# Optimization experiments

Hardware: AMD Instinct MI355X
Metric: run time of the kernel (lower is better)

Reference implementation:

```python
import jax, jax.numpy as jnp
import numpy as np

B, D, H, L = 2, 1024, 16, 4
BLK = 16                 # block_size == max_text_tokens
MT, MF = 16, 2032        # max_text_tokens, max_font_tokens
S = MT + MF              # 2048
NB = S // BLK            # 128 blocks
V = 490                  # font_vocab_size
HD = D // H              # 64
WIN = 30                 # 3*max_glyph_tokens/block_size = 3*160/16
NGLOB, NRAND = 1, 2      # BigBird global / random blocks
SOS = 0.42


def _make_layout():
    # Deterministic BigBird block layout per head: [H, NB, NB] bool
    rng = np.random.default_rng(0)
    layout = np.zeros((H, NB, NB), dtype=bool)
    layout[:, :NGLOB, :] = True          # global rows
    layout[:, :, :NGLOB] = True          # global cols
    for i in range(NB):                  # sliding window
        layout[:, i, max(0, i - WIN // 2):min(NB, i + WIN // 2 + 1)] = True
    for h in range(H):                   # random blocks
        for i in range(NB):
            layout[h, i, rng.choice(NB, size=NRAND, replace=False)] = True
    return jnp.asarray(layout)


def setup_inputs() -> dict:
    key = jax.random.key(0)
    ks = jax.random.split(key, 16)
    p = lambda k, shape: (0.02 * jax.random.normal(k, shape)).astype(jnp.float32)
    return {
        "text_embeddings": jax.random.normal(ks[0], (B, MT, D), jnp.float32),
        "font_embeddings": jax.random.normal(ks[1], (B, MF, D), jnp.float32),
        "layout": _make_layout(),
        "Wq": p(ks[2], (L, D, D)), "bq": jnp.zeros((L, D), jnp.float32),
        "Wk": p(ks[3], (L, D, D)), "bk": jnp.zeros((L, D), jnp.float32),
        "Wv": p(ks[4], (L, D, D)), "bv": jnp.zeros((L, D), jnp.float32),
        "Wo": p(ks[5], (L, D, D)), "bo": jnp.zeros((L, D), jnp.float32),
        "ln1_g": jnp.ones((L, D), jnp.float32), "ln1_b": jnp.zeros((L, D), jnp.float32),
        "ln2_g": jnp.ones((L, D), jnp.float32), "ln2_b": jnp.zeros((L, D), jnp.float32),
        "W1": p(ks[6], (L, D, 4 * D)), "b1": jnp.zeros((L, 4 * D), jnp.float32),
        "W2": p(ks[7], (L, 4 * D, D)), "b2": jnp.zeros((L, D), jnp.float32),
        "lnf_g": jnp.ones((D,), jnp.float32), "lnf_b": jnp.zeros((D,), jnp.float32),
        "Wout": p(ks[8], (D, V)),
    }


def _ln(x, g, b, eps=1e-5):
    mu = x.mean(-1, keepdims=True)
    var = ((x - mu) ** 2).mean(-1, keepdims=True)
    return (x - mu) * jax.lax.rsqrt(var + eps) * g + b


def _forward(text_embeddings, font_embeddings, layout, Wq, bq, Wk, bk, Wv, bv, Wo, bo,
             ln1_g, ln1_b, ln2_g, ln2_b, W1, b1, W2, b2, lnf_g, lnf_b, Wout):
    sos = jnp.full((B, 1, D), SOS, text_embeddings.dtype)
    x = jnp.concatenate([sos, text_embeddings, font_embeddings[:, :-1, :]], axis=1)  # [B,S,D]
    # token-level mask = block-sparse BigBird layout AND causal -> [H,S,S]
    tok_mask = jnp.repeat(jnp.repeat(layout, BLK, axis=1), BLK, axis=2)
    tok_mask = tok_mask & jnp.tril(jnp.ones((S, S), bool))[None]
    neg = jnp.asarray(-1e9, x.dtype)
    scale = jnp.asarray(1.0 / np.sqrt(HD), x.dtype)

    def layer(x, p):
        wq, bq_, wk, bk_, wv, bv_, wo, bo_, g1, gb1, g2, gb2, w1, bb1, w2, bb2 = p
        q = (x @ wq + bq_).reshape(B, S, H, HD).transpose(0, 2, 1, 3)
        k = (x @ wk + bk_).reshape(B, S, H, HD).transpose(0, 2, 1, 3)
        v = (x @ wv + bv_).reshape(B, S, H, HD).transpose(0, 2, 1, 3)
        scores = jnp.einsum('bhqd,bhkd->bhqk', q, k) * scale
        scores = jnp.where(tok_mask[None], scores, neg)
        probs = jax.nn.softmax(scores, axis=-1)
        a = jnp.einsum('bhqk,bhkd->bhqd', probs, v).transpose(0, 2, 1, 3).reshape(B, S, D)
        a = a @ wo + bo_
        x = _ln(x + a, g1, gb1)                                   # post-norm residual
        m = jax.nn.gelu(x @ w1 + bb1, approximate=False) @ w2 + bb2  # dropout=eval no-op
        x = _ln(x + m, g2, gb2)
        return x, None

    params = (Wq, bq, Wk, bk, Wv, bv, Wo, bo, ln1_g, ln1_b, ln2_g, ln2_b, W1, b1, W2, b2)
    x, _ = jax.lax.scan(jax.checkpoint(layer), x, params)
    logits = _ln(x, lnf_g, lnf_b) @ Wout                          # [B,S,V]
    return logits[:, :MT, :], logits[:, MT:, :]


def reference(text_embeddings, font_embeddings, layout, Wq, bq, Wk, bk, Wv, bv, Wo, bo,
              ln1_g, ln1_b, ln2_g, ln2_b, W1, b1, W2, b2, lnf_g, lnf_b, Wout):
    return _forward(text_embeddings, font_embeddings, layout, Wq, bq, Wk, bk, Wv, bv, Wo, bo,
                    ln1_g, ln1_b, ln2_g, ln2_b, W1, b1, W2, b2, lnf_g, lnf_b, Wout)
```

## Files before the change

### kernel.cpp

```cpp
#include <hip/hip_runtime.h>
#include <hip/hip_bf16.h>
#include <math.h>


typedef __hip_bfloat16 bf16;
typedef __attribute__((ext_vector_type(8))) short bf16x8;
typedef __attribute__((ext_vector_type(8))) unsigned short us8;
typedef __attribute__((ext_vector_type(4))) unsigned short us4;
typedef __attribute__((ext_vector_type(4))) float f32x4;
typedef __attribute__((ext_vector_type(8))) _Float16 f16x8;

#define S_LEN 2048
#define D_MODEL 1024
#define NBLK 128
#define NHEAD 16
#define BATCH 2
#define M_ROWS 4096
#define VOCAB 490

__device__ __forceinline__ float ldw(const void* p, size_t i, bool bf) {
    return bf ? __bfloat162float(((const bf16*)p)[i]) : ((const float*)p)[i];
}
__device__ __forceinline__ bool is_bf(const unsigned* probe) {
    return probe[0] != 0x3F800000u;
}
__device__ __forceinline__ unsigned short f2b(float f) {
    union { float f; unsigned u; } x; x.f = f;
    return (unsigned short)((x.u + 0x7FFFu + ((x.u >> 16) & 1u)) >> 16);
}
__device__ __forceinline__ unsigned short f2h(float f) {
    union { _Float16 h; unsigned short u; } x; x.h = (_Float16)f;
    return x.u;
}
__device__ __forceinline__ unsigned packh(float a, float b) {
    return (unsigned)f2h(a) | ((unsigned)f2h(b) << 16);
}
__device__ __forceinline__ float gelu_exact(float v) {
    float z = fabsf(v) * 0.70710678118654752f;
    float t = __builtin_amdgcn_rcpf(fmaf(0.3275911f, z, 1.f));
    float p = t * fmaf(t, fmaf(t, fmaf(t, fmaf(t, 1.061405429f, -1.453152027f),
                  1.421413741f), -0.284496736f), 0.254829592f);
    float er = 1.f - p * __expf(-z * z);
    er = copysignf(er, v);
    return 0.5f * v * (1.f + er);
}

__global__ __launch_bounds__(256) void norm_layout_kernel(
    const unsigned char* __restrict__ lraw, unsigned char* __restrict__ mask)
{
    int i = blockIdx.x * 256 + threadIdx.x;
    bool bytes_mode = (lraw[1] == 1);
    unsigned char v;
    if (bytes_mode) v = lraw[i] ? 1 : 0;
    else            v = ((const unsigned*)lraw)[i] ? 1 : 0;
    mask[i] = v;
}

__global__ __launch_bounds__(256) void build_x_kernel(
    const void* __restrict__ text, const void* __restrict__ font,
    float* __restrict__ x, unsigned short* __restrict__ xb,
    const unsigned* __restrict__ probe)
{
    bool bf = is_bf(probe);
    size_t idx = (size_t)blockIdx.x * 256 + threadIdx.x;
    int d = (int)(idx & 1023);
    int s = (int)((idx >> 10) & 2047);
    int b = (int)(idx >> 21);
    float v;
    if (s == 0)       v = bf ? 0.419921875f : 0.42f;
    else if (s <= 16) v = ldw(text, ((size_t)(b * 16 + (s - 1))) * 1024 + d, bf);
    else              v = ldw(font, ((size_t)(b * 2032 + (s - 17))) * 1024 + d, bf);
    x[idx] = v;
    xb[idx] = f2b(v);
}

__device__ __forceinline__ void transw_tile(
    const void* W, size_t wOff, unsigned short* Wt,
    int K, int N, int k0, int n0, int t, bool bf)
{
    __shared__ unsigned short tile[32][36];
    int r  = t >> 3;
    int c4 = (t & 7) * 4;
    int n = n0 + c4;
    us4 tv;
    if (n + 4 <= N) {
        if (bf) {
            tv = *(const us4*)((const unsigned short*)W + wOff + (size_t)(k0 + r) * N + n);
        } else {
            float4 f = *(const float4*)((const float*)W + wOff + (size_t)(k0 + r) * N + n);
            tv = (us4){ f2b(f.x), f2b(f.y), f2b(f.z), f2b(f.w) };
        }
    } else {
        #pragma unroll
        for (int i = 0; i < 4; ++i)
            tv[i] = (n + i < N) ? f2b(ldw(W, wOff + (size_t)(k0 + r) * N + n + i, bf))
                                : (unsigned short)0;
    }
    *(us4*)(&tile[r][c4]) = tv;
    __syncthreads();
    int rn = t >> 3;
    int k4 = (t & 7) * 4;
    us4 ov = { tile[k4 + 0][rn], tile[k4 + 1][rn], tile[k4 + 2][rn], tile[k4 + 3][rn] };
    *(us4*)(&Wt[(size_t)(n0 + rn) * K + k0 + k4]) = ov;
}

__global__ __launch_bounds__(256) void transw_kernel(
    const void* __restrict__ W, size_t wOff, unsigned short* __restrict__ Wt,
    int K, int N, const unsigned* __restrict__ probe)
{
    transw_tile(W, wOff, Wt, K, N, blockIdx.x * 32, blockIdx.y * 32,
                threadIdx.x, is_bf(probe));
}

__global__ __launch_bounds__(256) void transw_layer_kernel(
    const void* __restrict__ Wq, const void* __restrict__ Wk,
    const void* __restrict__ Wv, const void* __restrict__ Wo,
    const void* __restrict__ W1, const void* __restrict__ W2,
    size_t wo4, size_t wo16, unsigned short* __restrict__ wt,
    const unsigned* __restrict__ probe)
{
    bool bf = is_bf(probe);
    const size_t M1 = (size_t)1 << 20;
    int bx = blockIdx.x, by = blockIdx.y, z = blockIdx.z;
    if (z == 0) {
        int wsel = by >> 5;
        const void* W = wsel == 0 ? Wq : (wsel == 1 ? Wk : (wsel == 2 ? Wv : Wo));
        transw_tile(W, wo4, wt + (size_t)wsel * M1, 1024, 1024,
                    bx * 32, (by & 31) * 32, threadIdx.x, bf);
    } else if (z == 1) {
        transw_tile(W1, wo16, wt + 4 * M1, 1024, 4096,
                    bx * 32, by * 32, threadIdx.x, bf);
    } else {
        transw_tile(W2, wo16, wt + 8 * M1, 4096, 1024,
                    by * 32, bx * 32, threadIdx.x, bf);
    }
}

__global__ __launch_bounds__(512) void gemm_kernel(
    const unsigned short* __restrict__ Ab,
    const unsigned short* __restrict__ Wt, size_t wtStride,
    const void* __restrict__ b0, const void* __restrict__ b1p, const void* __restrict__ b2p,
    size_t bOff,
    float* __restrict__ C0, float* __restrict__ C1, float* __restrict__ C2,
    void* __restrict__ Cb0, void* __restrict__ Cb1, void* __restrict__ Cb2,
    float* __restrict__ Cp,
    int M, int N, int K, int act, int outmode, const unsigned* __restrict__ probe)
{
    bool bf = is_bf(probe);
    __shared__ __align__(16) unsigned short As[2][128 * 64];
    __shared__ __align__(16) unsigned short Bs[2][128 * 64];

    int t    = threadIdx.x;
    int lane = t & 63;
    int wid  = t >> 6;
    int wm   = wid >> 2;
    int wn   = wid & 3;

    int gx  = gridDim.x;
    int gy  = gridDim.y;
    int bid = blockIdx.y * gx + blockIdx.x;
    int mi, ni;
    if (gy == 32 && (gx & 3) == 0) {
        int xcd = bid & 7, c = bid >> 3;
        int xr = xcd >> 2, xc = xcd & 3;
        int rw = gx >> 2;
        mi = xr * 16 + (c & 15);
        ni = xc * rw + (c >> 4);
    } else {
        int nwg = gx * gy;
        int swz = (bid & 7) * (nwg >> 3) + (bid >> 3);
        mi = swz / gx; ni = swz % gx;
    }
    int m0  = mi * 128;
    int n0t = ni * 128;
    int sel = n0t / N;
    int n0  = n0t - sel * N;
    int zz  = blockIdx.z;
    int Kit = K / gridDim.z;
    int kbase = zz * Kit;

    const void* bias = sel == 0 ? b0 : (sel == 1 ? b1p : b2p);
    float* C         = sel == 0 ? C0 : (sel == 1 ? C1 : C2);
    void* Cb         = sel == 0 ? Cb0 : (sel == 1 ? Cb1 : Cb2);
    const unsigned short* Wtb = Wt + (size_t)sel * wtStride;
    const bool vtr = (outmode == 3 && sel == 2);

    f32x4 acc[4][2];
    #pragma unroll
    for (int i = 0; i < 4; i++)
        #pragma unroll
        for (int j = 0; j < 2; j++)
            acc[i][j] = (f32x4){0.f, 0.f, 0.f, 0.f};

    const int fm = lane & 15;

    auto stageA = [&](int bb, int kt) {
        int k0 = kbase + (kt << 6);
        #pragma unroll
        for (int c = 0; c < 2; ++c) {
            int p    = (wid * 2 + c) * 64 + lane;
            int row  = p >> 3;
            int cp   = p & 7;
            int csrc = cp ^ (row & 7);
            const unsigned short* src = Ab + (size_t)(m0 + row) * K + k0 + csrc * 8;
            unsigned short* dst = &As[bb][(wid * 2 + c) * 512];
            __builtin_amdgcn_global_load_lds(
                (const __attribute__((address_space(1))) unsigned int*)src,
                (__attribute__((address_space(3))) unsigned int*)dst, 16, 0, 0);
        }
    };
    auto stageB = [&](int bb, int kt) {
        int k0 = kbase + (kt << 6);
        #pragma unroll
        for (int c = 0; c < 2; ++c) {
            int p    = (wid * 2 + c) * 64 + lane;
            int row  = p >> 3;
            int cp   = p & 7;
            int csrc = cp ^ (row & 7);
            const unsigned short* src = Wtb + (size_t)(n0 + row) * K + k0 + csrc * 8;
            unsigned short* dst = &Bs[bb][(wid * 2 + c) * 512];
            __builtin_amdgcn_global_load_lds(
                (const __attribute__((address_space(1))) unsigned int*)src,
                (__attribute__((address_space(3))) unsigned int*)dst, 16, 0, 0);
        }
    };
    auto compute = [&](int bb) {
        #pragma unroll
        for (int kk = 0; kk < 2; ++kk) {
            int cq = kk * 4 + (lane >> 4);
            bf16x8 af[4], bfr[2];
            #pragma unroll
            for (int i = 0; i < 4; ++i) {
                int r = wm * 64 + i * 16 + fm;
                af[i] = *(const bf16x8*)(&As[bb][r * 64 + (cq ^ (r & 7)) * 8]);
            }
            #pragma unroll
            for (int j = 0; j < 2; ++j) {
                int n = wn * 32 + j * 16 + fm;
                bfr[j] = *(const bf16x8*)(&Bs[bb][n * 64 + (cq ^ (n & 7)) * 8]);
            }
            #pragma unroll
            for (int i = 0; i < 4; ++i)
                #pragma unroll
                for (int j = 0; j < 2; ++j)
                    acc[i][j] = __builtin_amdgcn_mfma_f32_16x16x32_bf16(
                        af[i], bfr[j], acc[i][j], 0, 0, 0);
        }
    };

    int nt = Kit >> 6;
    stageA(0, 0);
    stageB(0, 0);
    __syncthreads();

    for (int kt = 0; kt < nt; ++kt) {
        int cur = kt & 1;
        bool more = (kt + 1) < nt;
        if (more) { stageA(cur ^ 1, kt + 1); stageB(cur ^ 1, kt + 1); }
        compute(cur);
        __syncthreads();
    }

    int rq = (lane >> 4) * 4;
    #pragma unroll
    for (int j = 0; j < 2; ++j) {
        int n = n0 + wn * 32 + j * 16 + fm;
        if (n >= N) continue;
        float bv = (bias && zz == 0) ? ldw(bias, bOff + n, bf) : 0.f;
        #pragma unroll
        for (int i = 0; i < 4; ++i) {
            int mb = m0 + wm * 64 + i * 16 + rq;
            if (zz > 0) {
                #pragma unroll
                for (int r = 0; r < 4; ++r)
                    Cp[(size_t)(mb + r) * N + n] = acc[i][j][r];
                continue;
            }
            if (vtr) {
                us4 o;
                #pragma unroll
                for (int r = 0; r < 4; ++r) o[r] = f2h(acc[i][j][r] + bv);
                int bb2 = mb >> 11, s0 = mb & 2047, hh = n >> 6, dd = n & 63;
                *(us4*)(&((unsigned short*)Cb)[((((size_t)(bb2 * 16 + hh)) * 64 + dd) << 11) + s0]) = o;
                continue;
            }
            #pragma unroll
            for (int r = 0; r < 4; ++r) {
                int m = mb + r;
                float v = acc[i][j][r] + bv;
                if (act == 1) v = gelu_exact(v);
                if (outmode == 0) {
                    C[(size_t)m * N + n] = v;
                } else if (outmode == 2) {
                    ((unsigned short*)Cb)[(size_t)m * N + n] = f2b(v);
                } else if (outmode == 3) {
                    ((unsigned short*)Cb)[(size_t)m * N + n] = f2h(v);
                } else {
                    int b = m >> 11;
                    int s = m & 2047;
                    size_t dst;
                    if (s < 16) dst = ((size_t)(b * 16 + s)) * N + n;
                    else        dst = (size_t)(BATCH * 16) * N + ((size_t)(b * 2032 + (s - 16))) * N + n;
                    if (bf) ((unsigned short*)Cb)[dst] = f2b(v);
                    else    ((float*)Cb)[dst] = v;
                }
            }
        }
    }
}

__global__ __launch_bounds__(256) void attn_kernel(
    const unsigned short* __restrict__ q16, const unsigned short* __restrict__ k16,
    const unsigned short* __restrict__ v16t, const unsigned char* __restrict__ mask,
    unsigned short* __restrict__ ab)
{
    int qgrp = (S_LEN / 64 - 1) - blockIdx.x;
    int h = blockIdx.y, b = blockIdx.z;

    __shared__ __align__(16) unsigned short ksd[64 * 64];
    __shared__ __align__(16) unsigned short vst[64 * 64];
    __shared__ unsigned char cflag[33];
    __shared__ unsigned char aclist[33];
    __shared__ int nac;

    int t = threadIdx.x, lane = t & 63, w = t >> 6;
    int qb = qgrp * 4 + w;
    const int fm = lane & 15, rq = lane >> 4;

    const unsigned char* mrow0 = mask + ((size_t)h * NBLK) * NBLK;

    if (t <= qgrp) {
        int jc = t;
        bool f = false;
        #pragma unroll
        for (int mb = 0; mb < 4; ++mb) {
            int j = jc * 4 + mb;
            #pragma unroll
            for (int ww = 0; ww < 4; ++ww) {
                int qq = qgrp * 4 + ww;
                f = f || ((j <= qq) && mrow0[qq * NBLK + j]);
            }
        }
        cflag[jc] = f ? 1 : 0;
    }
    __syncthreads();
    if (t == 0) {
        int n = 0;
        for (int jc = 0; jc <= qgrp; ++jc)
            if (cflag[jc]) aclist[n++] = (unsigned char)jc;
        nac = n;
    }

    int qrow = qb * 16 + fm;
    size_t qbase = ((size_t)(b * S_LEN + qrow)) * D_MODEL + h * 64;
    f16x8 qf0 = *(const f16x8*)(q16 + qbase + rq * 8);
    f16x8 qf1 = *(const f16x8*)(q16 + qbase + 32 + rq * 8);

    f32x4 O[4];
    #pragma unroll
    for (int c = 0; c < 4; ++c) O[c] = (f32x4){0.f, 0.f, 0.f, 0.f};
    float m_run = -1e30f, l_run = 0.f;
    const f16x8 hzero = (f16x8){0,0,0,0,0,0,0,0};

    __syncthreads();
    int nacl = nac;

    const int srow = t >> 2;
    const int sg   = (t & 3) * 2;
    const size_t vtbase = ((size_t)(b * NHEAD + h) * 64) * S_LEN;
    us8 kr0, kr1, vr0, vr1;

    auto loadKV = [&](int jc) {
        size_t kb = ((size_t)(b * S_LEN + jc * 64 + srow)) * D_MODEL + h * 64 + sg * 8;
        kr0 = *(const us8*)(k16 + kb);
        kr1 = *(const us8*)(k16 + kb + 8);
        size_t vb_ = vtbase + (size_t)srow * S_LEN + jc * 64 + sg * 8;
        vr0 = *(const us8*)(v16t + vb_);
        vr1 = *(const us8*)(v16t + vb_ + 8);
    };
    auto writeKV = [&]() {
        int p0 = (sg) ^ (srow & 7), p1 = (sg + 1) ^ (srow & 7);
        *(us8*)(&ksd[srow * 64 + p0 * 8]) = kr0;
        *(us8*)(&ksd[srow * 64 + p1 * 8]) = kr1;
        *(us8*)(&vst[srow * 64 + p0 * 8]) = vr0;
        *(us8*)(&vst[srow * 64 + p1 * 8]) = vr1;
    };

    if (nacl > 0) loadKV(aclist[0]);

    for (int ci = 0; ci < nacl; ++ci) {
        int jc = aclist[ci];
        __syncthreads();
        writeKV();
        if (ci + 1 < nacl) loadKV(aclist[ci + 1]);
        __syncthreads();

        #pragma unroll
        for (int mb = 0; mb < 4; ++mb) {
            int j = jc * 4 + mb;
            bool actv = (j <= qb) && mrow0[qb * NBLK + j];
            if (!actv) continue;

            int krow = mb * 16 + fm;
            f16x8 kf0 = *(const f16x8*)(&ksd[krow * 64 + ((0 * 4 + rq) ^ (krow & 7)) * 8]);
            f16x8 kf1 = *(const f16x8*)(&ksd[krow * 64 + ((1 * 4 + rq) ^ (krow & 7)) * 8]);
            f32x4 st = (f32x4){0.f, 0.f, 0.f, 0.f};
            st = __builtin_amdgcn_mfma_f32_16x16x32_f16(kf0, qf0, st, 0, 0, 0);
            st = __builtin_amdgcn_mfma_f32_16x16x32_f16(kf1, qf1, st, 0, 0, 0);

            float s[4];
            #pragma unroll
            for (int r = 0; r < 4; ++r) {
                s[r] = st[r] * 0.125f;
                if (j == qb && (rq * 4 + r) > fm) s[r] = -1e30f;
            }
            float bm = fmaxf(fmaxf(s[0], s[1]), fmaxf(s[2], s[3]));
            bm = fmaxf(bm, __shfl_xor(bm, 16));
            bm = fmaxf(bm, __shfl_xor(bm, 32));
            bool noresc = __all(bm <= m_run + 8.f);
            float mx = noresc ? m_run : fmaxf(m_run, bm);
            float p[4]; float ls = 0.f;
            #pragma unroll
            for (int r = 0; r < 4; ++r) {
                p[r] = (s[r] < -1e29f) ? 0.f : __expf(s[r] - mx);
                ls += p[r];
            }
            ls += __shfl_xor(ls, 16);
            ls += __shfl_xor(ls, 32);

            unsigned ph01 = packh(p[0], p[1]), ph23 = packh(p[2], p[3]);
            int s0 = fm + (((rq & 1) * 2) << 4);
            int s1 = s0 + 16;
            unsigned w0 = __shfl(ph01, s0), w1 = __shfl(ph23, s0);
            unsigned w2 = __shfl(ph01, s1), w3 = __shfl(ph23, s1);
            union { unsigned u[4]; f16x8 v; } pcv;
            pcv.u[0] = w0; pcv.u[1] = w1; pcv.u[2] = w2; pcv.u[3] = w3;
            f16x8 pa = (rq < 2) ? pcv.v : hzero;

            if (noresc) {
                l_run += ls;
            } else {
                float al = __expf(m_run - mx);
                l_run = l_run * al + ls;
                m_run = mx;
                float al0 = __shfl(al, rq * 4 + 0), al1 = __shfl(al, rq * 4 + 1);
                float al2 = __shfl(al, rq * 4 + 2), al3 = __shfl(al, rq * 4 + 3);
                #pragma unroll
                for (int c = 0; c < 4; ++c) {
                    O[c][0] *= al0; O[c][1] *= al1; O[c][2] *= al2; O[c][3] *= al3;
                }
            }
            #pragma unroll
            for (int c = 0; c < 4; ++c) {
                f16x8 vb = hzero;
                if (rq < 2) {
                    int vrow = c * 16 + fm;
                    vb = *(const f16x8*)(&vst[vrow * 64 + ((mb * 2 + rq) ^ (vrow & 7)) * 8]);
                }
                O[c] = __builtin_amdgcn_mfma_f32_16x16x32_f16(pa, vb, O[c], 0, 0, 0);
            }
        }
    }

    float li0 = 1.f / __shfl(l_run, rq * 4 + 0);
    float li1 = 1.f / __shfl(l_run, rq * 4 + 1);
    float li2 = 1.f / __shfl(l_run, rq * 4 + 2);
    float li3 = 1.f / __shfl(l_run, rq * 4 + 3);
    size_t obase = ((size_t)(b * S_LEN + qb * 16)) * D_MODEL + h * 64;
    #pragma unroll
    for (int c = 0; c < 4; ++c) {
        ab[obase + (size_t)(rq * 4 + 0) * D_MODEL + c * 16 + fm] = f2b(O[c][0] * li0);
        ab[obase + (size_t)(rq * 4 + 1) * D_MODEL + c * 16 + fm] = f2b(O[c][1] * li1);
        ab[obase + (size_t)(rq * 4 + 2) * D_MODEL + c * 16 + fm] = f2b(O[c][2] * li2);
        ab[obase + (size_t)(rq * 4 + 3) * D_MODEL + c * 16 + fm] = f2b(O[c][3] * li3);
    }
}

__global__ __launch_bounds__(256) void add_ln_kernel(
    const float* __restrict__ xin, const float* __restrict__ res,
    const float* __restrict__ res2,
    float* __restrict__ xout, unsigned short* __restrict__ bfout,
    const void* __restrict__ g, size_t gOff,
    const void* __restrict__ bt, size_t bOff, const unsigned* __restrict__ probe)
{
    bool bf = is_bf(probe);
    int row = blockIdx.x;
    int t = threadIdx.x;
    __shared__ float red[4];

    float4 xv = ((const float4*)(xin + (size_t)row * D_MODEL))[t];
    if (res) {
        float4 rv = ((const float4*)(res + (size_t)row * D_MODEL))[t];
        xv.x += rv.x; xv.y += rv.y; xv.z += rv.z; xv.w += rv.w;
    }
    if (res2) {
        float4 rv = ((const float4*)(res2 + (size_t)row * D_MODEL))[t];
        xv.x += rv.x; xv.y += rv.y; xv.z += rv.z; xv.w += rv.w;
    }
    float s = xv.x + xv.y + xv.z + xv.w;
    for (int off = 32; off > 0; off >>= 1) s += __shfl_down(s, off);
    if ((t & 63) == 0) red[t >> 6] = s;
    __syncthreads();
    float mu = (red[0] + red[1] + red[2] + red[3]) * (1.f / 1024.f);
    __syncthreads();

    float d0 = xv.x - mu, d1 = xv.y - mu, d2 = xv.z - mu, d3 = xv.w - mu;
    float s2 = d0 * d0 + d1 * d1 + d2 * d2 + d3 * d3;
    for (int off = 32; off > 0; off >>= 1) s2 += __shfl_down(s2, off);
    if ((t & 63) == 0) red[t >> 6] = s2;
    __syncthreads();
    float var = (red[0] + red[1] + red[2] + red[3]) * (1.f / 1024.f);
    float rstd = rsqrtf(var + 1e-5f);

    int dbase = t * 4;
    float4 ov;
    ov.x = d0 * rstd * ldw(g, gOff + dbase + 0, bf) + ldw(bt, bOff + dbase + 0, bf);
    ov.y = d1 * rstd * ldw(g, gOff + dbase + 1, bf) + ldw(bt, bOff + dbase + 1, bf);
    ov.z = d2 * rstd * ldw(g, gOff + dbase + 2, bf) + ldw(bt, bOff + dbase + 2, bf);
    ov.w = d3 * rstd * ldw(g, gOff + dbase + 3, bf) + ldw(bt, bOff + dbase + 3, bf);
    ((float4*)(xout + (size_t)row * D_MODEL))[t] = ov;
    if (bfout) {
        us4 bv = { f2b(ov.x), f2b(ov.y), f2b(ov.z), f2b(ov.w) };
        *(us4*)(bfout + (size_t)row * D_MODEL + dbase) = bv;
    }
}

extern "C" void kernel_launch(void* const* d_in, const int* in_sizes, int n_in,
                              void* d_out, int out_size, void* d_ws, size_t ws_size,
                              hipStream_t stream) {
    const void* text  = d_in[0];
    const void* font  = d_in[1];
    const unsigned char* lraw = (const unsigned char*)d_in[2];
    const void* Wq    = d_in[3];
    const void* bq    = d_in[4];
    const void* Wk    = d_in[5];
    const void* bk    = d_in[6];
    const void* Wv    = d_in[7];
    const void* bv    = d_in[8];
    const void* Wo    = d_in[9];
    const void* bo_   = d_in[10];
    const void* ln1g  = d_in[11];
    const void* ln1b  = d_in[12];
    const void* ln2g  = d_in[13];
    const void* ln2b  = d_in[14];
    const void* W1    = d_in[15];
    const void* b1    = d_in[16];
    const void* W2    = d_in[17];
    const void* b2    = d_in[18];
    const void* lnfg  = d_in[19];
    const void* lnfb  = d_in[20];
    const void* Wout  = d_in[21];
    const unsigned* probe = (const unsigned*)d_in[11];

    const size_t Q = (size_t)M_ROWS * D_MODEL;
    float* ws = (float*)d_ws;
    float* x  = ws;
    float* G0 = ws + Q;
    unsigned short* q16 = (unsigned short*)(ws + 2 * Q);
    unsigned short* k16 = q16 + Q;
    unsigned short* v16 = k16 + Q;
    unsigned short* hb  = (unsigned short*)(ws + 2 * Q);
    unsigned short* xb  = (unsigned short*)(ws + 4 * Q);
    unsigned short* ab  = (unsigned short*)(ws + 4 * Q + Q / 2);
    unsigned char* mask = (unsigned char*)(ws + 5 * Q);
    unsigned short* wt  = (unsigned short*)((char*)d_ws + 5 * Q * 4 + 262144);

    const size_t M1 = (size_t)1 << 20;
    const size_t baseEnd = 5 * Q * 4 + 262144 + 12 * M1 * 2;
    bool canSplit = ws_size >= baseEnd + Q * 4;
    float* part = (float*)((char*)d_ws + baseEnd);

    norm_layout_kernel<<<(NHEAD * NBLK * NBLK) / 256, 256, 0, stream>>>(lraw, mask);
    build_x_kernel<<<(BATCH * S_LEN * D_MODEL) / 256, 256, 0, stream>>>(text, font, x, xb, probe);

    dim3 gQKV(3 * D_MODEL / 128, M_ROWS / 128);
    dim3 gD(D_MODEL / 128, M_ROWS / 128, canSplit ? 2 : 1);
    dim3 gF(4 * D_MODEL / 128, M_ROWS / 128);
    dim3 gV((VOCAB + 127) / 128, M_ROWS / 128);

    const size_t MSZ = M1;
    const float* r2 = canSplit ? part : nullptr;

    for (int l = 0; l < 4; l++) {
        size_t wo  = (size_t)l * D_MODEL * D_MODEL;
        size_t bo1 = (size_t)l * D_MODEL;
        size_t w1o = (size_t)l * D_MODEL * 4 * D_MODEL;
        size_t b1o = (size_t)l * 4 * D_MODEL;

        transw_layer_kernel<<<dim3(32, 128, 3), 256, 0, stream>>>(
            Wq, Wk, Wv, Wo, W1, W2, wo, w1o, wt, probe);

        gemm_kernel<<<gQKV, 512, 0, stream>>>(xb, wt, MSZ, bq, bk, bv, bo1,
                                              nullptr, nullptr, nullptr, q16, k16, v16,
                                              nullptr,
                                              M_ROWS, D_MODEL, D_MODEL, 0, 3, probe);
        attn_kernel<<<dim3(S_LEN / 64, NHEAD, BATCH), 256, 0, stream>>>(
            q16, k16, v16, mask, ab);
        gemm_kernel<<<gD, 512, 0, stream>>>(ab, wt + 3 * MSZ, 0, bo_, bo_, bo_, bo1,
                                            G0, G0, G0, nullptr, nullptr, nullptr,
                                            part,
                                            M_ROWS, D_MODEL, D_MODEL, 0, 0, probe);
        add_ln_kernel<<<M_ROWS, 256, 0, stream>>>(x, G0, r2, x, xb, ln1g, bo1, ln1b, bo1, probe);

        gemm_kernel<<<gF, 512, 0, stream>>>(xb, wt + 4 * MSZ, 0, b1, b1, b1, b1o,
                                            nullptr, nullptr, nullptr, hb, hb, hb,
                                            nullptr,
                                            M_ROWS, 4 * D_MODEL, D_MODEL, 1, 2, probe);
        gemm_kernel<<<gD, 512, 0, stream>>>(hb, wt + 8 * MSZ, 0, b2, b2, b2, bo1,
                                            G0, G0, G0, nullptr, nullptr, nullptr,
                                            part,
                                            M_ROWS, D_MODEL, 4 * D_MODEL, 0, 0, probe);
        add_ln_kernel<<<M_ROWS, 256, 0, stream>>>(x, G0, r2, x, xb, ln2g, bo1, ln2b, bo1, probe);
    }

    add_ln_kernel<<<M_ROWS, 256, 0, stream>>>(x, nullptr, nullptr, G0, ab, lnfg, 0, lnfb, 0, probe);
    transw_kernel<<<dim3(32, 16), 256, 0, stream>>>(Wout, 0, wt, D_MODEL, VOCAB, probe);
    gemm_kernel<<<gV, 512, 0, stream>>>(ab, wt, 0, nullptr, nullptr, nullptr, 0,
                                        nullptr, nullptr, nullptr, d_out, d_out, d_out,
                                        nullptr,
                                        M_ROWS, VOCAB, D_MODEL, 0, 1, probe);
}
```

Baseline: 1.231 ms.

## Fuse weight transposes into LayerNorm and build kernels to cut launches

Merges the layout-normalisation kernel into build_x and moves the first layer's weight transpose plus the Wout transpose into one launch before the layer loop. For later layers, the next layer's weight transpose is fused with the post-FFN add+LayerNorm into one grid, with the z==3 slice handling LN rows. The aim is fewer kernel launches and letting the transpose overlap with LN work. The cost is a larger workspace for the separate Wout transpose buffer, and it relies on the LN output not overlapping the transposed weight region.

```diff
diff --git a/kernel.cpp b/kernel.cpp
--- a/kernel.cpp
+++ b/kernel.cpp
@@ -45,22 +45,65 @@
     return 0.5f * v * (1.f + er);
 }
 
-__global__ __launch_bounds__(256) void norm_layout_kernel(
-    const unsigned char* __restrict__ lraw, unsigned char* __restrict__ mask)
-{
-    int i = blockIdx.x * 256 + threadIdx.x;
-    bool bytes_mode = (lraw[1] == 1);
-    unsigned char v;
-    if (bytes_mode) v = lraw[i] ? 1 : 0;
-    else            v = ((const unsigned*)lraw)[i] ? 1 : 0;
-    mask[i] = v;
+__device__ __forceinline__ void add_ln_row(
+    const float* xin, const float* res, const float* res2,
+    float* xout, unsigned short* bfout,
+    const void* g, size_t gOff, const void* bt, size_t bOff,
+    int row, int t, bool bf)
+{
+    __shared__ float red[4];
+    float4 xv = ((const float4*)(xin + (size_t)row * D_MODEL))[t];
+    if (res) {
+        float4 rv = ((const float4*)(res + (size_t)row * D_MODEL))[t];
+        xv.x += rv.x; xv.y += rv.y; xv.z += rv.z; xv.w += rv.w;
+    }
+    if (res2) {
+        float4 rv = ((const float4*)(res2 + (size_t)row * D_MODEL))[t];
+        xv.x += rv.x; xv.y += rv.y; xv.z += rv.z; xv.w += rv.w;
+    }
+    float s = xv.x + xv.y + xv.z + xv.w;
+    for (int off = 32; off > 0; off >>= 1) s += __shfl_down(s, off);
+    if ((t & 63) == 0) red[t >> 6] = s;
+    __syncthreads();
+    float mu = (red[0] + red[1] + red[2] + red[3]) * (1.f / 1024.f);
+    __syncthreads();
+
+    float d0 = xv.x - mu, d1 = xv.y - mu, d2 = xv.z - mu, d3 = xv.w - mu;
+    float s2 = d0 * d0 + d1 * d1 + d2 * d2 + d3 * d3;
+    for (int off = 32; off > 0; off >>= 1) s2 += __shfl_down(s2, off);
+    if ((t & 63) == 0) red[t >> 6] = s2;
+    __syncthreads();
+    float var = (red[0] + red[1] + red[2] + red[3]) * (1.f / 1024.f);
+    float rstd = rsqrtf(var + 1e-5f);
+
+    int dbase = t * 4;
+    float4 ov;
+    ov.x = d0 * rstd * ldw(g, gOff + dbase + 0, bf) + ldw(bt, bOff + dbase + 0, bf);
+    ov.y = d1 * rstd * ldw(g, gOff + dbase + 1, bf) + ldw(bt, bOff + dbase + 1, bf);
+    ov.z = d2 * rstd * ldw(g, gOff + dbase + 2, bf) + ldw(bt, bOff + dbase + 2, bf);
+    ov.w = d3 * rstd * ldw(g, gOff + dbase + 3, bf) + ldw(bt, bOff + dbase + 3, bf);
+    ((float4*)(xout + (size_t)row * D_MODEL))[t] = ov;
+    if (bfout) {
+        us4 bv = { f2b(ov.x), f2b(ov.y), f2b(ov.z), f2b(ov.w) };
+        *(us4*)(bfout + (size_t)row * D_MODEL + dbase) = bv;
+    }
 }
 
 __global__ __launch_bounds__(256) void build_x_kernel(
     const void* __restrict__ text, const void* __restrict__ font,
     float* __restrict__ x, unsigned short* __restrict__ xb,
+    const unsigned char* __restrict__ lraw, unsigned char* __restrict__ mask,
     const unsigned* __restrict__ probe)
 {
+    if (blockIdx.x >= 16384) {
+        int i = (blockIdx.x - 16384) * 256 + threadIdx.x;
+        bool bytes_mode = (lraw[1] == 1);
+        unsigned char v;
+        if (bytes_mode) v = lraw[i] ? 1 : 0;
+        else            v = ((const unsigned*)lraw)[i] ? 1 : 0;
+        mask[i] = v;
+        return;
+    }
     bool bf = is_bf(probe);
     size_t idx = (size_t)blockIdx.x * 256 + threadIdx.x;
     int d = (int)(idx & 1023);
@@ -104,18 +147,11 @@
     *(us4*)(&Wt[(size_t)(n0 + rn) * K + k0 + k4]) = ov;
 }
 
-__global__ __launch_bounds__(256) void transw_kernel(
-    const void* __restrict__ W, size_t wOff, unsigned short* __restrict__ Wt,
-    int K, int N, const unsigned* __restrict__ probe)
-{
-    transw_tile(W, wOff, Wt, K, N, blockIdx.x * 32, blockIdx.y * 32,
-                threadIdx.x, is_bf(probe));
-}
-
 __global__ __launch_bounds__(256) void transw_layer_kernel(
     const void* __restrict__ Wq, const void* __restrict__ Wk,
     const void* __restrict__ Wv, const void* __restrict__ Wo,
     const void* __restrict__ W1, const void* __restrict__ W2,
+    const void* __restrict__ Wout,
     size_t wo4, size_t wo16, unsigned short* __restrict__ wt,
     const unsigned* __restrict__ probe)
 {
@@ -130,9 +166,45 @@
     } else if (z == 1) {
         transw_tile(W1, wo16, wt + 4 * M1, 1024, 4096,
                     bx * 32, by * 32, threadIdx.x, bf);
-    } else {
+    } else if (z == 2) {
         transw_tile(W2, wo16, wt + 8 * M1, 4096, 1024,
                     by * 32, bx * 32, threadIdx.x, bf);
+    } else {
+        if (!Wout || by >= 16) return;
+        transw_tile(Wout, 0, wt + 12 * M1, 1024, VOCAB,
+                    bx * 32, by * 32, threadIdx.x, bf);
+    }
+}
+
+__global__ __launch_bounds__(256) void lnw_kernel(
+    const float* __restrict__ xin, const float* __restrict__ res,
+    const float* __restrict__ res2,
+    float* __restrict__ xout, unsigned short* __restrict__ bfout,
+    const void* __restrict__ g, size_t gOff,
+    const void* __restrict__ bt, size_t bOff,
+    const void* __restrict__ Wq, const void* __restrict__ Wk,
+    const void* __restrict__ Wv, const void* __restrict__ Wo,
+    const void* __restrict__ W1, const void* __restrict__ W2,
+    size_t wo4, size_t wo16, unsigned short* __restrict__ wt,
+    const unsigned* __restrict__ probe)
+{
+    bool bf = is_bf(probe);
+    const size_t M1 = (size_t)1 << 20;
+    int bx = blockIdx.x, by = blockIdx.y, z = blockIdx.z;
+    if (z == 0) {
+        int wsel = by >> 5;
+        const void* W = wsel == 0 ? Wq : (wsel == 1 ? Wk : (wsel == 2 ? Wv : Wo));
+        transw_tile(W, wo4, wt + (size_t)wsel * M1, 1024, 1024,
+                    bx * 32, (by & 31) * 32, threadIdx.x, bf);
+    } else if (z == 1) {
+        transw_tile(W1, wo16, wt + 4 * M1, 1024, 4096,
+                    bx * 32, by * 32, threadIdx.x, bf);
+    } else if (z == 2) {
+        transw_tile(W2, wo16, wt + 8 * M1, 4096, 1024,
+                    by * 32, bx * 32, threadIdx.x, bf);
+    } else {
+        add_ln_row(xin, res, res2, xout, bfout, g, gOff, bt, bOff,
+                   by * 32 + bx, threadIdx.x, bf);
     }
 }
 
@@ -483,46 +555,8 @@
     const void* __restrict__ g, size_t gOff,
     const void* __restrict__ bt, size_t bOff, const unsigned* __restrict__ probe)
 {
-    bool bf = is_bf(probe);
-    int row = blockIdx.x;
-    int t = threadIdx.x;
-    __shared__ float red[4];
-
-    float4 xv = ((const float4*)(xin + (size_t)row * D_MODEL))[t];
-    if (res) {
-        float4 rv = ((const float4*)(res + (size_t)row * D_MODEL))[t];
-        xv.x += rv.x; xv.y += rv.y; xv.z += rv.z; xv.w += rv.w;
-    }
-    if (res2) {
-        float4 rv = ((const float4*)(res2 + (size_t)row * D_MODEL))[t];
-        xv.x += rv.x; xv.y += rv.y; xv.z += rv.z; xv.w += rv.w;
-    }
-    float s = xv.x + xv.y + xv.z + xv.w;
-    for (int off = 32; off > 0; off >>= 1) s += __shfl_down(s, off);
-    if ((t & 63) == 0) red[t >> 6] = s;
-    __syncthreads();
-    float mu = (red[0] + red[1] + red[2] + red[3]) * (1.f / 1024.f);
-    __syncthreads();
-
-    float d0 = xv.x - mu, d1 = xv.y - mu, d2 = xv.z - mu, d3 = xv.w - mu;
-    float s2 = d0 * d0 + d1 * d1 + d2 * d2 + d3 * d3;
-    for (int off = 32; off > 0; off >>= 1) s2 += __shfl_down(s2, off);
-    if ((t & 63) == 0) red[t >> 6] = s2;
-    __syncthreads();
-    float var = (red[0] + red[1] + red[2] + red[3]) * (1.f / 1024.f);
-    float rstd = rsqrtf(var + 1e-5f);
-
-    int dbase = t * 4;
-    float4 ov;
-    ov.x = d0 * rstd * ldw(g, gOff + dbase + 0, bf) + ldw(bt, bOff + dbase + 0, bf);
-    ov.y = d1 * rstd * ldw(g, gOff + dbase + 1, bf) + ldw(bt, bOff + dbase + 1, bf);
-    ov.z = d2 * rstd * ldw(g, gOff + dbase + 2, bf) + ldw(bt, bOff + dbase + 2, bf);
-    ov.w = d3 * rstd * ldw(g, gOff + dbase + 3, bf) + ldw(bt, bOff + dbase + 3, bf);
-    ((float4*)(xout + (size_t)row * D_MODEL))[t] = ov;
-    if (bfout) {
-        us4 bv = { f2b(ov.x), f2b(ov.y), f2b(ov.z), f2b(ov.w) };
-        *(us4*)(bfout + (size_t)row * D_MODEL + dbase) = bv;
-    }
+    add_ln_row(xin, res, res2, xout, bfout, g, gOff, bt, bOff,
+               blockIdx.x, threadIdx.x, is_bf(probe));
 }
 
 extern "C" void kernel_launch(void* const* d_in, const int* in_sizes, int n_in,
@@ -566,12 +600,13 @@
     unsigned short* wt  = (unsigned short*)((char*)d_ws + 5 * Q * 4 + 262144);
 
     const size_t M1 = (size_t)1 << 20;
-    const size_t baseEnd = 5 * Q * 4 + 262144 + 12 * M1 * 2;
+    const size_t baseEnd = 5 * Q * 4 + 262144 + (12 * M1 + (M1 >> 1)) * 2;
     bool canSplit = ws_size >= baseEnd + Q * 4;
     float* part = (float*)((char*)d_ws + baseEnd);
 
-    norm_layout_kernel<<<(NHEAD * NBLK * NBLK) / 256, 256, 0, stream>>>(lraw, mask);
-    build_x_kernel<<<(BATCH * S_LEN * D_MODEL) / 256, 256, 0, stream>>>(text, font, x, xb, probe);
+    build_x_kernel<<<17408, 256, 0, stream>>>(text, font, x, xb, lraw, mask, probe);
+    transw_layer_kernel<<<dim3(32, 128, 4), 256, 0, stream>>>(
+        Wq, Wk, Wv, Wo, W1, W2, Wout, 0, 0, wt, probe);
 
     dim3 gQKV(3 * D_MODEL / 128, M_ROWS / 128);
     dim3 gD(D_MODEL / 128, M_ROWS / 128, canSplit ? 2 : 1);
@@ -582,13 +617,10 @@
     const float* r2 = canSplit ? part : nullptr;
 
     for (int l = 0; l < 4; l++) {
-        size_t wo  = (size_t)l * D_MODEL * D_MODEL;
         size_t bo1 = (size_t)l * D_MODEL;
-        size_t w1o = (size_t)l * D_MODEL * 4 * D_MODEL;
         size_t b1o = (size_t)l * 4 * D_MODEL;
-
-        transw_layer_kernel<<<dim3(32, 128, 3), 256, 0, stream>>>(
-            Wq, Wk, Wv, Wo, W1, W2, wo, w1o, wt, probe);
+        size_t won = (size_t)(l + 1) * D_MODEL * D_MODEL;
+        size_t w1n = (size_t)(l + 1) * D_MODEL * 4 * D_MODEL;
 
         gemm_kernel<<<gQKV, 512, 0, stream>>>(xb, wt, MSZ, bq, bk, bv, bo1,
                                               nullptr, nullptr, nullptr, q16, k16, v16,
@@ -610,12 +642,18 @@
                                             G0, G0, G0, nullptr, nullptr, nullptr,
                                             part,
                                             M_ROWS, D_MODEL, 4 * D_MODEL, 0, 0, probe);
-        add_ln_kernel<<<M_ROWS, 256, 0, stream>>>(x, G0, r2, x, xb, ln2g, bo1, ln2b, bo1, probe);
+        if (l < 3) {
+            lnw_kernel<<<dim3(32, 128, 4), 256, 0, stream>>>(
+                x, G0, r2, x, xb, ln2g, bo1, ln2b, bo1,
+                Wq, Wk, Wv, Wo, W1, W2, won, w1n, wt, probe);
+        } else {
+            add_ln_kernel<<<M_ROWS, 256, 0, stream>>>(x, G0, r2, x, xb,
+                                                      ln2g, bo1, ln2b, bo1, probe);
+        }
     }
 
     add_ln_kernel<<<M_ROWS, 256, 0, stream>>>(x, nullptr, nullptr, G0, ab, lnfg, 0, lnfb, 0, probe);
-    transw_kernel<<<dim3(32, 16), 256, 0, stream>>>(Wout, 0, wt, D_MODEL, VOCAB, probe);
-    gemm_kernel<<<gV, 512, 0, stream>>>(ab, wt, 0, nullptr, nullptr, nullptr, 0,
+    gemm_kernel<<<gV, 512, 0, stream>>>(ab, wt + 12 * MSZ, 0, nullptr, nullptr, nullptr, 0,
                                         nullptr, nullptr, nullptr, d_out, d_out, d_out,
                                         nullptr,
                                         M_ROWS, VOCAB, D_MODEL, 0, 1, probe);
```

New measurement: 1.227 ms, median of 2. About the same (-0.4%).
